# Performance work log

Hardware: AMD Instinct MI355X
Metric: run time of the kernel (lower is better)

Reference implementation:

```python
import jax, jax.numpy as jnp
import numpy as np

B, N_ENC, N_DEC = 32, 512, 512
IN_V, OUT_V = 2000, 2000
H, F, K, P = 256, 256, 5, 4  # P = |G| (indices < P are masked to 0 before embedding)
E_ENC, E_DEC = 128, 128


def setup_inputs() -> dict:
    key = jax.random.key(0)
    ks = jax.random.split(key, 16)
    s = lambda i, shape, scale=0.05: jax.random.normal(ks[i], shape, jnp.float32) * scale
    return dict(
        xs_idx=jax.random.randint(ks[0], (B, N_ENC), 0, IN_V),
        ys_idx=jax.random.randint(ks[1], (B, N_DEC), 0, OUT_V),
        gembed_W=s(2, (IN_V, F)),
        gconv_W=s(3, (K, F, F)),
        gdecode_W=s(4, (F, OUT_V)),
        enc_embed=s(5, (IN_V, E_ENC)),
        dec_embed=s(6, (OUT_V, E_DEC)),
        enc_Wih=s(7, (4 * H, E_ENC)),
        enc_Whh=s(8, (4 * H, H)),
        enc_b=jnp.zeros((4 * H,), jnp.float32),
        dec_Wih=s(9, (4 * H, E_DEC)),
        dec_Whh=s(10, (4 * H, H)),
        dec_b=jnp.zeros((4 * H,), jnp.float32),
        T=jax.random.uniform(ks[11], (H, 2 * H), jnp.float32, -0.5, 0.5),
    )


def _lstm(x, Wih, Whh, b, h0, c0):
    # x: (B, T, D); PyTorch gate order i, f, g, o
    def step(carry, xt):
        h, c = carry
        z = xt @ Wih.T + h @ Whh.T + b
        i, f, g, o = jnp.split(z, 4, axis=-1)
        c = jax.nn.sigmoid(f) * c + jax.nn.sigmoid(i) * jnp.tanh(g)
        h = jax.nn.sigmoid(o) * jnp.tanh(c)
        return (h, c), h
    (hT, cT), hs = jax.lax.scan(step, (h0, c0), jnp.swapaxes(x, 0, 1))
    return jnp.swapaxes(hs, 0, 1), hT, cT


def reference(xs_idx, ys_idx, gembed_W, gconv_W, gdecode_W, enc_embed, dec_embed,
              enc_Wih, enc_Whh, enc_b, dec_Wih, dec_Whh, dec_b, T):
    # --- G-equivariant stack: per-encoder-position distribution over output vocab ---
    e = jnp.tanh(gembed_W[xs_idx])  # (B, Ne, F)
    c = jax.lax.conv_general_dilated(e, gconv_W, (1,), 'SAME',
                                     dimension_numbers=('NWC', 'WIO', 'NWC'))
    probs = jax.nn.softmax(jnp.tanh(c) @ gdecode_W, axis=-1)  # (B, Ne, V)
    # encoder_scores[b, i, j] = probs[b, i, ys[b, j]]
    idx = jnp.broadcast_to(ys_idx[:, None, :], (probs.shape[0], probs.shape[1], ys_idx.shape[1]))
    encoder_scores = jnp.take_along_axis(probs, idx, axis=2)  # (B, Ne, Nd)

    # --- invariant LSTM encoder (indices < |G| masked to 0) ---
    xm = jnp.where(xs_idx < P, 0, xs_idx)
    x_embed = enc_embed[xm]  # (B, Ne, E)
    z = jnp.zeros((x_embed.shape[0], H), jnp.float32)
    henc, hT, cT = _lstm(x_embed, enc_Wih, enc_Whh, enc_b, z, z)
    hback, _, _ = _lstm(jnp.flip(x_embed, axis=1), enc_Wih, enc_Whh, enc_b, z, z)
    hback = jnp.flip(hback, axis=1)

    # --- decoder LSTM, initialized with encoder final state ---
    ym = jnp.where(ys_idx < P, 0, ys_idx)
    y_embed = dec_embed[ym]
    out, _, _ = _lstm(y_embed, dec_Wih, dec_Whh, dec_b, hT, cT)
    h_dec = jnp.concatenate([henc[:, -1:, :], out], axis=1)[:, :-1, :]  # (B, Nd, H)
    h_enc = jnp.concatenate([henc, hback], axis=2)  # (B, Ne, 2H)

    # --- bilinear alignment scores: eij[b, i, j] = h_dec[b, j] . (T @ h_enc[b, i]) ---
    Th = jnp.einsum('he,bie->bih', T, h_enc)           # (B, Ne, H)
    eij = jnp.einsum('bjh,bih->bij', h_dec, Th)        # (B, Ne, Nd)
    align = jax.nn.softmax(eij, axis=1)                # softmax over encoder positions

    p = jnp.sum(jnp.log(jnp.sum(encoder_scores * align, axis=1)), axis=1)  # (B,)
    return -jnp.sum(p)
```

## Files before the change

kernel.cpp:

```cpp
#include <hip/hip_runtime.h>

typedef _Float16 f16;
typedef _Float16 f16x2 __attribute__((ext_vector_type(2)));
typedef _Float16 f16x4 __attribute__((ext_vector_type(4)));
typedef _Float16 f16x8 __attribute__((ext_vector_type(8)));
typedef float    f32x4 __attribute__((ext_vector_type(4)));
typedef int      i32x4 __attribute__((ext_vector_type(4)));
typedef unsigned int u32;
typedef unsigned short u16;

#define DEVI static __device__ __forceinline__

static constexpr int LDT = 40;
static constexpr int LDA = 264;

DEVI float sigf(float x){ return 1.f/(1.f + __expf(-x)); }
DEVI float tanh_c(float x){
  x = fminf(fmaxf(x, -15.f), 15.f);
  float e = __expf(2.f*x);
  return (e - 1.f)/(e + 1.f);
}
DEVI float sig_f(float x){ return __builtin_amdgcn_rcpf(1.f + __expf(-x)); }
DEVI float tanh_f(float x){ return 1.f - 2.f*__builtin_amdgcn_rcpf(1.f + __expf(2.f*x)); }
DEVI float wmax16(float v){
  #pragma unroll
  for (int m=1;m<16;m<<=1) v = fmaxf(v, __shfl_xor(v, m, 64));
  return v;
}
DEVI float wsum16(float v){
  #pragma unroll
  for (int m=1;m<16;m<<=1) v += __shfl_xor(v, m, 64);
  return v;
}
DEVI f16x8 frag_ld(const f16* p){ return *(const f16x8*)p; }
DEVI void stage_tileh(int t256, const f16* src, int ld, f16* dst){
  int row = t256>>2, qq = t256&3;
  *(f16x8*)(dst + row*LDT + qq*8) = *(const f16x8*)(src + (size_t)row*ld + qq*8);
}
#define ZERO4(acc) { f32x4 _z = {0.f,0.f,0.f,0.f}; acc[0]=_z; acc[1]=_z; acc[2]=_z; acc[3]=_z; }

DEVI void gemm64h(int t256, const f16* A, int lda, const f16* Bm, int ldb, int K,
                  f16* lA, f16* lB, f32x4 acc[4]){
  const int lane = t256 & 63, wv = t256 >> 6;
  const int l15 = lane & 15, kq = lane >> 4;
  for (int k0=0; k0<K; k0+=32){
    __syncthreads();
    stage_tileh(t256, A + k0, lda, lA);
    stage_tileh(t256, Bm + k0, ldb, lB);
    __syncthreads();
    f16x8 af = frag_ld(lA + (16*wv + l15)*LDT + kq*8);
    #pragma unroll
    for (int nt=0; nt<4; nt++){
      f16x8 bf = frag_ld(lB + (16*nt + l15)*LDT + kq*8);
      acc[nt] = __builtin_amdgcn_mfma_f32_16x16x32_f16(af, bf, acc[nt], 0,0,0);
    }
  }
}

__global__ void k_cvt(const float* __restrict__ s, f16* __restrict__ d, int n){
  int i = blockIdx.x*256 + threadIdx.x;
  if (i < n) d[i] = (f16)s[i];
}
__global__ void k_gconvT(const float* __restrict__ s, f16* __restrict__ d){
  int id = blockIdx.x;
  int fo = threadIdx.x;
  d[(size_t)fo*1280 + id] = (f16)s[(size_t)id*256 + fo];
}
__global__ void k_gdecT(const float* __restrict__ s, f16* __restrict__ d){
  int v = blockIdx.x, f = threadIdx.x;
  f16 val = (f16)0.f;
  if (v < 2000) val = (f16)s[(size_t)f*2000 + v];
  d[(size_t)v*256 + f] = val;
}
__global__ void k_epad(const int* __restrict__ xs, const float* __restrict__ gemb, f16* __restrict__ epad){
  int id = blockIdx.x;
  int f = threadIdx.x;
  int b = id / 516, p = id % 516;
  float v = 0.f;
  if (p >= 2 && p < 514){ int idx = xs[b*512 + p - 2]; v = tanh_c(gemb[(size_t)idx*256 + f]); }
  epad[(size_t)id*256 + f] = (f16)v;
}
__global__ void k_embx(const int* __restrict__ xs, const int* __restrict__ ys,
                       const float* __restrict__ eemb, const float* __restrict__ demb,
                       f16* __restrict__ xo, f16* __restrict__ yo){
  int id = blockIdx.x; int f = threadIdx.x;
  bool dec = id >= 32*512; int id2 = dec ? id - 32*512 : id;
  int idx = dec ? ys[id2] : xs[id2];
  if (idx < 4) idx = 0;
  const float* src = (dec ? demb : eemb) + (size_t)idx*128;
  (dec ? yo : xo)[(size_t)id2*128 + f] = (f16)src[f];
}

__global__ void k_wmax(const float* __restrict__ Whh, u32* __restrict__ ws){
  int i = (blockIdx.x*256 + threadIdx.x)*4;
  float m = 0.f;
  #pragma unroll
  for (int j=0;j<4;j++) m = fmaxf(m, fabsf(Whh[i+j]));
  #pragma unroll
  for (int d=1; d<64; d<<=1) m = fmaxf(m, __shfl_xor(m, d, 64));
  if ((threadIdx.x & 63) == 0) atomicMax(ws, __float_as_uint(m));
}
__global__ void k_wq8(const float* __restrict__ Whh, const u32* __restrict__ ws,
                      i32x4* __restrict__ Wq){
  const int bid = blockIdx.x;
  const int l = threadIdx.x;
  const int kt = bid & 3, t8 = (bid >> 2) & 7, w = bid >> 5;
  const int r15 = l & 15;
  const int u4 = r15 >> 2, g = r15 & 3;
  const int unit = w*32 + t8*4 + u4;
  const int row = g*256 + unit;
  const int k0  = kt*64 + (l >> 4)*16;
  const float scale = 127.f / __uint_as_float(ws[0]);
  int dw[4];
  #pragma unroll
  for (int d=0; d<4; d++){
    u32 acc = 0;
    #pragma unroll
    for (int j=0; j<4; j++){
      float q = __builtin_rintf(Whh[(size_t)row*256 + k0 + d*4 + j] * scale);
      int qi = (int)fminf(fmaxf(q, -127.f), 127.f);
      acc |= ((u32)qi & 0xffu) << (8*j);
    }
    dw[d] = (int)acc;
  }
  i32x4 v = { dw[0], dw[1], dw[2], dw[3] };
  Wq[(size_t)bid*64 + l] = v;
}

__global__ __launch_bounds__(256,4) void k_conv(const f16* __restrict__ epad, const f16* __restrict__ gcT, f16* __restrict__ tf){
  __shared__ f16 lA[64*LDT], lB[64*LDT];
  const int m0 = blockIdx.x*64, n0 = blockIdx.y*64;
  const int b = m0 >> 9, n = m0 & 511;
  f32x4 acc[4]; ZERO4(acc);
  gemm64h(threadIdx.x, epad + ((size_t)b*516 + n)*256, 256, gcT + (size_t)n0*1280, 1280, 1280, lA, lB, acc);
  const int lane=threadIdx.x&63, wv=threadIdx.x>>6, l15=lane&15, kq=lane>>4;
  #pragma unroll
  for (int nt=0;nt<4;nt++)
    #pragma unroll
    for (int r=0;r<4;r++)
      tf[(size_t)(m0 + 16*wv + 4*kq + r)*256 + n0 + nt*16 + l15] = (f16)tanh_c(acc[nt][r]);
}

DEVI void ku_body(int t256, int m0, int n0, const f16* X, const f16* Wih,
                  const float* bias, f16* U, f16* lA, f16* lB){
  f32x4 acc[4]; ZERO4(acc);
  gemm64h(t256, X + (size_t)m0*128, 128, Wih + (size_t)n0*128, 128, 128, lA, lB, acc);
  const int lane=t256&63, wv=t256>>6, l15=lane&15, kq=lane>>4;
  #pragma unroll
  for (int nt=0;nt<4;nt++){
    int n = n0 + nt*16 + l15;
    float bv = bias[n];
    int cnew = (n & 255)*4 + (n >> 8);
    #pragma unroll
    for (int r=0;r<4;r++)
      U[(size_t)(m0 + 16*wv + 4*kq + r)*1024 + cnew] = (f16)(acc[nt][r] + bv);
  }
}

__global__ __launch_bounds__(256,4) void k_u(const f16* __restrict__ X, const f16* __restrict__ Wih,
                                             const float* __restrict__ bias, f16* __restrict__ U){
  __shared__ f16 lA[64*LDT], lB[64*LDT];
  ku_body(threadIdx.x, blockIdx.x*64, blockIdx.y*64, X, Wih, bias, U, lA, lB);
}

DEVI void th_body(int t256, int m0, int n0, const f16* henh, const f16* Tf, f16* Th,
                  f16* lA, f16* lB){
  f32x4 acc[4]; ZERO4(acc);
  gemm64h(t256, henh + (size_t)m0*512, 512, Tf + (size_t)n0*512, 512, 512, lA, lB, acc);
  const int lane=t256&63, wv=t256>>6, l15=lane&15, kq=lane>>4;
  #pragma unroll
  for (int nt=0;nt<4;nt++)
    #pragma unroll
    for (int r=0;r<4;r++)
      Th[(size_t)(m0 + 16*wv + 4*kq + r)*256 + n0 + nt*16 + l15] = (f16)acc[nt][r];
}

DEVI void pass1_body(int tid, int mt, int ns, const f16* tf, const f16* gdT,
                     float* mxp, float* sep, f16* lA, f16* lB2, float* mxs2, float* ses2){
  const int half = tid >> 8, t256 = tid & 255;
  const int lane = tid & 63, wv = t256 >> 6, l15 = lane & 15, kq = lane >> 4;
  f16* lB = lB2 + half*(64*LDT);
  {
    const f16* A = tf + (size_t)mt*64*256;
    int row = tid >> 3, c8 = tid & 7;
    #pragma unroll
    for (int q=0;q<4;q++)
      *(f16x8*)(lA + row*LDA + c8*32 + q*8) = *(const f16x8*)(A + (size_t)row*256 + c8*32 + q*8);
  }
  if (t256 < 64){ mxs2[half*64 + t256] = -1e30f; ses2[half*64 + t256] = 0.f; }
  __syncthreads();
  for (int nci=0; nci<4; nci++){
    const int nc = half*4 + nci;
    const int nbase = ns*512 + nc*64;
    const f16* Bm = gdT + (size_t)nbase*256;
    f32x4 acc[4]; ZERO4(acc);
    for (int k0=0; k0<256; k0+=32){
      __syncthreads();
      stage_tileh(t256, Bm + k0, 256, lB);
      __syncthreads();
      f16x8 af = frag_ld(lA + (16*wv + l15)*LDA + k0 + kq*8);
      #pragma unroll
      for (int nt=0; nt<4; nt++){
        f16x8 bf = frag_ld(lB + (16*nt + l15)*LDT + kq*8);
        acc[nt] = __builtin_amdgcn_mfma_f32_16x16x32_f16(af, bf, acc[nt], 0,0,0);
      }
    }
    #pragma unroll
    for (int r=0;r<4;r++){
      float av[4]; float cm = -1e30f;
      #pragma unroll
      for (int nt=0;nt<4;nt++){
        int gcol = nbase + nt*16 + l15;
        float a = (gcol < 2000) ? acc[nt][r] : -1e30f;
        av[nt] = a; cm = fmaxf(cm, a);
      }
      cm = wmax16(cm);
      int rr = half*64 + 16*wv + 4*kq + r;
      float old = mxs2[rr];
      float nm = fmaxf(old, cm);
      float ss = 0.f;
      #pragma unroll
      for (int nt=0;nt<4;nt++) ss += __expf(av[nt] - nm);
      ss = wsum16(ss);
      if (l15 == 0){
        ses2[rr] = ses2[rr]*__expf(old - nm) + ss;
        mxs2[rr] = nm;
      }
    }
  }
  __syncthreads();
  if (tid < 64){
    float m0 = mxs2[tid], m1 = mxs2[64+tid];
    float nm = fmaxf(m0, m1);
    float se = ses2[tid]*__expf(m0-nm) + ses2[64+tid]*__expf(m1-nm);
    mxp[(size_t)ns*16384 + mt*64 + tid] = nm;
    sep[(size_t)ns*16384 + mt*64 + tid] = se;
  }
}

__global__ void k_comb1(const float* __restrict__ mxp, const float* __restrict__ sep,
                        float* __restrict__ mx, float* __restrict__ se){
  int m = blockIdx.x*256 + threadIdx.x;
  float best = -1e30f;
  #pragma unroll
  for (int k=0;k<4;k++) best = fmaxf(best, mxp[(size_t)k*16384 + m]);
  float s = 0.f;
  #pragma unroll
  for (int k=0;k<4;k++) s += sep[(size_t)k*16384 + m] * __expf(mxp[(size_t)k*16384 + m] - best);
  mx[m] = best; se[m] = s;
}

DEVI void pass2_body(int t256, int it, int jt, int b, const f16* tf, const f16* gdT,
                     const int* ys, const float* mx, const float* se, f16* scT,
                     f16* lA, f16* lB, int* jv){
  const int lane=t256&63, wv=t256>>6, l15=lane&15, kq=lane>>4;
  if (t256<64) jv[t256] = ys[b*512 + jt*64 + t256];
  const f16* A = tf + ((size_t)b*512 + it*64)*256;
  f32x4 acc[4]; ZERO4(acc);
  for (int k0=0;k0<256;k0+=32){
    __syncthreads();
    stage_tileh(t256, A + k0, 256, lA);
    { int row=t256>>2, qq=t256&3;
      *(f16x8*)(lB + row*LDT + qq*8) = *(const f16x8*)(gdT + (size_t)jv[row]*256 + k0 + qq*8); }
    __syncthreads();
    f16x8 af = frag_ld(lA + (16*wv+l15)*LDT + kq*8);
    #pragma unroll
    for (int nt=0;nt<4;nt++){
      f16x8 bf = frag_ld(lB + (16*nt+l15)*LDT + kq*8);
      acc[nt] = __builtin_amdgcn_mfma_f32_16x16x32_f16(af, bf, acc[nt], 0,0,0);
    }
  }
  float mxv[4], rsev[4];
  #pragma unroll
  for (int r=0;r<4;r++){
    int i_ = it*64 + 16*wv + 4*kq + r;
    mxv[r] = mx[b*512 + i_];
    rsev[r] = 1.f / se[b*512 + i_];
  }
  #pragma unroll
  for (int nt=0;nt<4;nt++){
    int j_ = jt*64 + nt*16 + l15;
    #pragma unroll
    for (int r=0;r<4;r++){
      int i_ = it*64 + 16*wv + 4*kq + r;
      scT[((size_t)b*512 + j_)*512 + i_] = (f16)(__expf(acc[nt][r] - mxv[r]) * rsev[r]);
    }
  }
}

__global__ __launch_bounds__(256,2) void k_final(const f16* __restrict__ hdec, const f16* __restrict__ Th,
                                                 const f16* __restrict__ scT,
                                                 float* __restrict__ pmx, float* __restrict__ pden, float* __restrict__ pnum){
  __shared__ f16 lA[64*LDA];
  __shared__ f16 lB[64*LDT];
  __shared__ float mx_s[64], den_s[64], num_s[64];
  const int is = blockIdx.x, jt = blockIdx.y, b = blockIdx.z;
  const int tid = threadIdx.x, lane=tid&63, wv=tid>>6, l15=lane&15, kq=lane>>4;
  {
    const f16* A = hdec + ((size_t)b*512 + jt*64)*256;
    int row = tid>>2, qq = tid&3;
    #pragma unroll
    for (int c=0;c<8;c++)
      *(f16x8*)(lA + row*LDA + c*32 + qq*8) = *(const f16x8*)(A + (size_t)row*256 + c*32 + qq*8);
  }
  if (tid<64){ mx_s[tid]=-1e30f; den_s[tid]=0.f; num_s[tid]=0.f; }
  __syncthreads();
  for (int ic=0; ic<4; ic++){
    const int i0 = is*256 + ic*64;
    const f16* Bm = Th + ((size_t)b*512 + i0)*256;
    f32x4 acc[4]; ZERO4(acc);
    for (int k0=0;k0<256;k0+=32){
      __syncthreads();
      stage_tileh(tid, Bm + k0, 256, lB);
      __syncthreads();
      f16x8 af = frag_ld(lA + (16*wv+l15)*LDA + k0 + kq*8);
      #pragma unroll
      for (int nt=0;nt<4;nt++){
        f16x8 bf = frag_ld(lB + (16*nt+l15)*LDT + kq*8);
        acc[nt] = __builtin_amdgcn_mfma_f32_16x16x32_f16(af, bf, acc[nt], 0,0,0);
      }
    }
    #pragma unroll
    for (int r=0;r<4;r++){
      int jl = 16*wv + 4*kq + r;
      float av[4]; float cm=-1e30f;
      #pragma unroll
      for (int nt=0;nt<4;nt++){ av[nt]=acc[nt][r]; cm=fmaxf(cm,av[nt]); }
      cm = wmax16(cm);
      float old = mx_s[jl], nm = fmaxf(old, cm);
      float ds=0.f, nsum=0.f;
      const size_t srow = ((size_t)b*512 + jt*64 + jl)*512;
      #pragma unroll
      for (int nt=0;nt<4;nt++){
        float e = __expf(av[nt]-nm);
        float sc = (float)scT[srow + i0 + nt*16 + l15];
        ds += e; nsum += sc*e;
      }
      ds = wsum16(ds); nsum = wsum16(nsum);
      if (l15==0){
        float fac = __expf(old-nm);
        den_s[jl] = den_s[jl]*fac + ds;
        num_s[jl] = num_s[jl]*fac + nsum;
        mx_s[jl] = nm;
      }
    }
  }
  __syncthreads();
  if (tid<64){
    size_t idx = (((size_t)b*512) + jt*64 + tid)*2 + is;
    pmx[idx]=mx_s[tid]; pden[idx]=den_s[tid]; pnum[idx]=num_s[tid];
  }
}

__global__ void k_comb2(const float* __restrict__ pmx, const float* __restrict__ pden,
                        const float* __restrict__ pnum, float* __restrict__ out){
  const int b = blockIdx.x, j = threadIdx.x;
  size_t base = ((size_t)b*512 + j)*2;
  float m0=pmx[base], m1=pmx[base+1];
  float m = fmaxf(m0,m1);
  float e0=__expf(m0-m), e1=__expf(m1-m);
  float den = pden[base]*e0 + pden[base+1]*e1;
  float num = pnum[base]*e0 + pnum[base+1]*e1;
  float lp = __logf(num) - __logf(den);
  __shared__ float red[512];
  red[j] = lp;
  __syncthreads();
  for (int st=256; st>0; st>>=1){ if (j<st) red[j]+=red[j+st]; __syncthreads(); }
  if (j==0) atomicAdd(out, -red[0]);
}

DEVI void lstm_core(char* smem, const f16* U, const i32x4* Wq, const u32* ws,
                    u16* hout, float* hTcT, u16* hdec0, int nsteps, int mode, int bid)
{
  char* h8b = smem;
  const int tid = threadIdx.x;
  const int lane = tid & 63, w = tid >> 6;
  const int l15 = lane & 15, kq = lane >> 4;
  const int s = l15 & 3, p = l15 >> 2;
  const int uA = w*32 + 8*p + kq;
  const int uB = uA + 4;

  int dir = 0, b0;
  if (mode == 0){ dir = bid >> 3; b0 = (bid & 7)*4; }
  else b0 = bid*4;

  const float zscale = __uint_as_float(ws[0]) * (1.f/(127.f*127.f));

  i32x4 aw[32];
  #pragma unroll
  for (int f=0; f<32; f++) aw[f] = Wq[(size_t)(w*32 + f)*64 + lane];

  float cA = 0.f, cB = 0.f;
  if (mode == 0){
    ((u32*)h8b)[tid] = 0u;
  } else {
    const float* hp = hTcT + (size_t)(b0+s)*512;
    float hA = hp[uA], hB = hp[uB];
    cA = hp[256 + uA]; cB = hp[256 + uB];
    h8b[((uA>>4)*4 + s)*16 + (uA&15)] = (char)(int)__builtin_rintf(hA*127.f);
    h8b[((uB>>4)*4 + s)*16 + (uB&15)] = (char)(int)__builtin_rintf(hB*127.f);
  }

  const f16* Urow = U + (size_t)(b0+s)*512*1024;
  f16x4 uvA, uvB;
  {
    int tp0 = dir ? (nsteps-1) : 0;
    uvA = *(const f16x4*)(Urow + (size_t)tp0*1024 + uA*4);
    uvB = *(const f16x4*)(Urow + (size_t)tp0*1024 + uB*4);
  }
  __syncthreads();

  int cur = 0;
  #pragma unroll 1
  for (int t=0; t<nsteps; ++t){
    const int tpos = dir ? (nsteps-1-t) : t;
    int tn = dir ? (nsteps-2-t >= 0 ? nsteps-2-t : 0) : (t+1 < nsteps ? t+1 : nsteps-1);
    f16x4 puA = *(const f16x4*)(Urow + (size_t)tn*1024 + uA*4);
    f16x4 puB = *(const f16x4*)(Urow + (size_t)tn*1024 + uB*4);

    const char* hc = h8b + cur*1024;
    i32x4 bf[4];
    #pragma unroll
    for (int kt=0; kt<4; kt++)
      bf[kt] = *(const i32x4*)(hc + ((kt*4 + kq)*4 + s)*16);

    i32x4 acc[8];
    #pragma unroll
    for (int t8=0; t8<8; t8++){
      i32x4 d = {0,0,0,0};
      #pragma unroll
      for (int kt=0; kt<4; kt++)
        d = __builtin_amdgcn_mfma_i32_16x16x64_i8(aw[t8*4+kt], bf[kt], d, 0,0,0);
      acc[t8] = d;
    }

    i32x4 vA, vB;
    #pragma unroll
    for (int e=0; e<4; e++){
      int x0 = (p&1) ? acc[2][e] : acc[0][e];
      int x1 = (p&1) ? acc[6][e] : acc[4][e];
      vA[e] = (p&2) ? x1 : x0;
      int y0 = (p&1) ? acc[3][e] : acc[1][e];
      int y1 = (p&1) ? acc[7][e] : acc[5][e];
      vB[e] = (p&2) ? y1 : y0;
    }

    float hA_, hB_;
    {
      float z0 = fmaf((float)vA[0], zscale, (float)uvA[0]);
      float z1 = fmaf((float)vA[1], zscale, (float)uvA[1]);
      float z2 = fmaf((float)vA[2], zscale, (float)uvA[2]);
      float z3 = fmaf((float)vA[3], zscale, (float)uvA[3]);
      cA = sig_f(z1)*cA + sig_f(z0)*tanh_f(z2);
      hA_ = sig_f(z3)*tanh_f(cA);
    }
    {
      float z0 = fmaf((float)vB[0], zscale, (float)uvB[0]);
      float z1 = fmaf((float)vB[1], zscale, (float)uvB[1]);
      float z2 = fmaf((float)vB[2], zscale, (float)uvB[2]);
      float z3 = fmaf((float)vB[3], zscale, (float)uvB[3]);
      cB = sig_f(z1)*cB + sig_f(z0)*tanh_f(z2);
      hB_ = sig_f(z3)*tanh_f(cB);
    }

    const int nxt = cur ^ 1;
    char* hn = h8b + nxt*1024;
    hn[((uA>>4)*4 + s)*16 + (uA&15)] = (char)(int)__builtin_rintf(hA_*127.f);
    hn[((uB>>4)*4 + s)*16 + (uB&15)] = (char)(int)__builtin_rintf(hB_*127.f);

    f16 fA = (f16)hA_, fB = (f16)hB_;
    if (mode == 0){
      u16* hr = hout + ((size_t)(b0+s)*512 + tpos)*512 + dir*256;
      hr[uA] = __builtin_bit_cast(u16, fA);
      hr[uB] = __builtin_bit_cast(u16, fB);
      if (!dir && t == nsteps-1){
        hdec0[(size_t)(b0+s)*512*256 + uA] = __builtin_bit_cast(u16, fA);
        hdec0[(size_t)(b0+s)*512*256 + uB] = __builtin_bit_cast(u16, fB);
        float* hp = hTcT + (size_t)(b0+s)*512;
        hp[uA] = hA_; hp[uB] = hB_;
        hp[256+uA] = cA; hp[256+uB] = cB;
      }
    } else {
      u16* hr = hout + ((size_t)(b0+s)*512 + (t+1))*256;
      hr[uA] = __builtin_bit_cast(u16, fA);
      hr[uB] = __builtin_bit_cast(u16, fB);
    }

    asm volatile("s_waitcnt lgkmcnt(0)" ::: "memory");
    __builtin_amdgcn_s_barrier();
    asm volatile("" ::: "memory");
    __builtin_amdgcn_sched_barrier(0);

    cur = nxt;
    uvA = puA; uvB = puB;
  }
}

__global__ __launch_bounds__(512,2) void k_mega_enc(
    const f16* __restrict__ Uenc, const i32x4* __restrict__ Wqe, const u32* __restrict__ wse,
    u16* __restrict__ henh, float* __restrict__ hTcT, u16* __restrict__ hdec0,
    const f16* __restrict__ tf, const f16* __restrict__ gdT,
    float* __restrict__ mxp, float* __restrict__ sep,
    const f16* __restrict__ yemb, const f16* __restrict__ Wihd,
    const float* __restrict__ db, f16* __restrict__ Udec)
{
  __shared__ __align__(16) char smem[45056];
  const int bid = blockIdx.x;
  const int tid = threadIdx.x;
  if (bid < 16){
    lstm_core(smem, Uenc, Wqe, wse, henh, hTcT, hdec0, 512, 0, bid);
  } else if (bid < 1040){
    int vb = bid - 16;
    int mt = vb >> 2;
    int ns = vb & 3;
    pass1_body(tid, mt, ns, tf, gdT, mxp, sep,
               (f16*)smem, (f16*)(smem + 33792), (float*)(smem + 44032), (float*)(smem + 44544));
  } else {
    int vb = bid - 1040;
    int half = tid >> 8, t256 = tid & 255;
    int vbm = vb >> 4, ny = vb & 15;
    int m0 = (vbm*2 + half)*64;
    int n0 = ny*64;
    char* base = smem + half*10240;
    ku_body(t256, m0, n0, yemb, Wihd, db, Udec, (f16*)base, (f16*)(base + 5120));
  }
}

__global__ __launch_bounds__(512,2) void k_mega_dec(
    const f16* __restrict__ Udec, const i32x4* __restrict__ Wqd, const u32* __restrict__ wsd,
    u16* __restrict__ hdec, float* __restrict__ hTcT,
    const f16* __restrict__ tf, const f16* __restrict__ gdT, const int* __restrict__ ys,
    const float* __restrict__ mx, const float* __restrict__ se, f16* __restrict__ scT,
    const f16* __restrict__ henh, const f16* __restrict__ Tf, f16* __restrict__ Th)
{
  __shared__ __align__(16) char smem[24576];
  const int bid = blockIdx.x;
  const int tid = threadIdx.x;
  if (bid < 8){
    lstm_core(smem, Udec, Wqd, wsd, hdec, hTcT, hdec, 511, 1, bid);
  } else if (bid < 1032){
    int vb = bid - 8;
    int half = tid >> 8, t256 = tid & 255;
    int b = vb >> 5, rem = vb & 31;
    int jt = rem >> 2, it = (rem & 3)*2 + half;
    char* base = smem + half*10496;
    pass2_body(t256, it, jt, b, tf, gdT, ys, mx, se, scT,
               (f16*)base, (f16*)(base + 5120), (int*)(base + 10240));
  } else {
    int vb = bid - 1032;
    int half = tid >> 8, t256 = tid & 255;
    int m0 = ((vb >> 2)*2 + half)*64;
    int n0 = (vb & 3)*64;
    char* base = smem + half*10240;
    th_body(t256, m0, n0, henh, Tf, Th, (f16*)base, (f16*)(base + 5120));
  }
}

extern "C" void kernel_launch(void* const* d_in, const int* in_sizes, int n_in,
                              void* d_out, int out_size, void* d_ws, size_t ws_size,
                              hipStream_t stream)
{
  (void)in_sizes; (void)n_in; (void)out_size;
  const int*   xs    = (const int*)d_in[0];
  const int*   ys    = (const int*)d_in[1];
  const float* gemb  = (const float*)d_in[2];
  const float* gconv = (const float*)d_in[3];
  const float* gdec  = (const float*)d_in[4];
  const float* eemb  = (const float*)d_in[5];
  const float* demb  = (const float*)d_in[6];
  const float* eWih  = (const float*)d_in[7];
  const float* eWhh  = (const float*)d_in[8];
  const float* eb    = (const float*)d_in[9];
  const float* dWih  = (const float*)d_in[10];
  const float* dWhh  = (const float*)d_in[11];
  const float* db    = (const float*)d_in[12];
  const float* Tm    = (const float*)d_in[13];

  char* wsb = (char*)d_ws;
  size_t off = 0;
  auto take = [&](size_t bytes)->char*{ char* p = wsb + off; off += (bytes + 255) & ~(size_t)255; return p; };
  f16* epad  = (f16*)take((size_t)32*516*256*2);
  f16* tf    = (f16*)take((size_t)32*512*256*2);
  f16* xemb  = (f16*)take((size_t)32*512*128*2);
  f16* yemb  = (f16*)take((size_t)32*512*128*2);
  f16* Uenc  = (f16*)take((size_t)32*512*1024*2);
  f16* Udec  = (f16*)take((size_t)32*512*1024*2);
  f16* henh  = (f16*)take((size_t)32*512*512*2);
  f16* hdec  = (f16*)take((size_t)32*512*256*2);
  f16* Th    = (f16*)take((size_t)32*512*256*2);
  f16* scT   = (f16*)take((size_t)32*512*512*2);
  float* mx  = (float*)take((size_t)16384*4);
  float* se  = (float*)take((size_t)16384*4);
  float* mxp = (float*)take((size_t)4*16384*4);
  float* sep = (float*)take((size_t)4*16384*4);
  float* pmx = (float*)take((size_t)32*512*2*4);
  float* pden= (float*)take((size_t)32*512*2*4);
  float* pnum= (float*)take((size_t)32*512*2*4);
  float* hTcT= (float*)take((size_t)32*512*4);
  f16* Wihe  = (f16*)take((size_t)1024*128*2);
  f16* Wihd  = (f16*)take((size_t)1024*128*2);
  f16* Tf    = (f16*)take((size_t)256*512*2);
  f16* gcT   = (f16*)take((size_t)256*1280*2);
  f16* gdT   = (f16*)take((size_t)2048*256*2);
  i32x4* Wq8e = (i32x4*)take((size_t)256*64*16);
  i32x4* Wq8d = (i32x4*)take((size_t)256*64*16);
  u32* wsc   = (u32*)take(8);
  if (off > ws_size) return;

  hipMemsetAsync(d_out, 0, sizeof(float), stream);
  hipMemsetAsync(wsc, 0, 8, stream);

  k_cvt<<<dim3(512),  256, 0, stream>>>(eWih, Wihe, 1024*128);
  k_cvt<<<dim3(512),  256, 0, stream>>>(dWih, Wihd, 1024*128);
  k_cvt<<<dim3(512),  256, 0, stream>>>(Tm,   Tf,   256*512);
  k_gconvT<<<dim3(1280), 256, 0, stream>>>(gconv, gcT);
  k_gdecT <<<dim3(2048), 256, 0, stream>>>(gdec, gdT);
  k_wmax<<<dim3(256), 256, 0, stream>>>(eWhh, wsc + 0);
  k_wmax<<<dim3(256), 256, 0, stream>>>(dWhh, wsc + 1);
  k_wq8<<<dim3(256), 64, 0, stream>>>(eWhh, wsc + 0, Wq8e);
  k_wq8<<<dim3(256), 64, 0, stream>>>(dWhh, wsc + 1, Wq8d);
  k_epad<<<dim3(32*516), 256, 0, stream>>>(xs, gemb, epad);
  k_embx<<<dim3(2*32*512), 128, 0, stream>>>(xs, ys, eemb, demb, xemb, yemb);

  k_conv<<<dim3(256,4), 256, 0, stream>>>(epad, gcT, tf);
  k_u<<<dim3(256,16), 256, 0, stream>>>(xemb, Wihe, eb, Uenc);

  k_mega_enc<<<dim3(3088), 512, 0, stream>>>(Uenc, Wq8e, wsc + 0, (u16*)henh, hTcT, (u16*)hdec,
                                             tf, gdT, mxp, sep, yemb, Wihd, db, Udec);
  k_comb1<<<dim3(64), 256, 0, stream>>>(mxp, sep, mx, se);

  k_mega_dec<<<dim3(1544), 512, 0, stream>>>(Udec, Wq8d, wsc + 1, (u16*)hdec, hTcT,
                                             tf, gdT, ys, mx, se, scT, henh, Tf, Th);

  k_final<<<dim3(2,8,32), 256, 0, stream>>>(hdec, Th, scT, pmx, pden, pnum);
  k_comb2<<<dim3(32), 512, 0, stream>>>(pmx, pden, pnum, (float*)d_out);
}
```

Baseline: 1.136 ms.

## Convert mega kernels' side work to persistent grid-stride workers

Both fused kernels now launch 512 blocks instead of thousands, and non-LSTM blocks loop over the pass1/ku and pass2/th work items with a grid stride. Blocks 256..271 (enc) and 256..263 (dec) exit early, apparently so the side workers avoid sharing CUs with the latency-critical LSTM blocks. The aim is to cut block dispatch overhead and interference with the serial LSTM recurrence. The cost is less parallel slack and possible tail imbalance among the fixed set of workers.

Result: no change. 1.134 ms (-0.2%).

```diff
diff --git a/kernel.cpp b/kernel.cpp
--- a/kernel.cpp
+++ b/kernel.cpp
@@ -509,20 +509,26 @@
   const int tid = threadIdx.x;
   if (bid < 16){
     lstm_core(smem, Uenc, Wqe, wse, henh, hTcT, hdec0, 512, 0, bid);
-  } else if (bid < 1040){
-    int vb = bid - 16;
-    int mt = vb >> 2;
-    int ns = vb & 3;
-    pass1_body(tid, mt, ns, tf, gdT, mxp, sep,
-               (f16*)smem, (f16*)(smem + 33792), (float*)(smem + 44032), (float*)(smem + 44544));
-  } else {
-    int vb = bid - 1040;
-    int half = tid >> 8, t256 = tid & 255;
-    int vbm = vb >> 4, ny = vb & 15;
-    int m0 = (vbm*2 + half)*64;
-    int n0 = ny*64;
-    char* base = smem + half*10240;
-    ku_body(t256, m0, n0, yemb, Wihd, db, Udec, (f16*)base, (f16*)(base + 5120));
+    return;
+  }
+  if (bid >= 256 && bid < 272) return;
+  const int w = (bid < 256) ? (bid - 16) : (bid - 32);
+  for (int v = w; v < 3072; v += 480){
+    __syncthreads();
+    if (v < 1024){
+      int mt = v >> 2;
+      int ns = v & 3;
+      pass1_body(tid, mt, ns, tf, gdT, mxp, sep,
+                 (f16*)smem, (f16*)(smem + 33792), (float*)(smem + 44032), (float*)(smem + 44544));
+    } else {
+      int vb = v - 1024;
+      int half = tid >> 8, t256 = tid & 255;
+      int vbm = vb >> 4, ny = vb & 15;
+      int m0 = (vbm*2 + half)*64;
+      int n0 = ny*64;
+      char* base = smem + half*10240;
+      ku_body(t256, m0, n0, yemb, Wihd, db, Udec, (f16*)base, (f16*)(base + 5120));
+    }
   }
 }
 
@@ -538,21 +544,27 @@
   const int tid = threadIdx.x;
   if (bid < 8){
     lstm_core(smem, Udec, Wqd, wsd, hdec, hTcT, hdec, 511, 1, bid);
-  } else if (bid < 1032){
-    int vb = bid - 8;
-    int half = tid >> 8, t256 = tid & 255;
-    int b = vb >> 5, rem = vb & 31;
-    int jt = rem >> 2, it = (rem & 3)*2 + half;
-    char* base = smem + half*10496;
-    pass2_body(t256, it, jt, b, tf, gdT, ys, mx, se, scT,
-               (f16*)base, (f16*)(base + 5120), (int*)(base + 10240));
-  } else {
-    int vb = bid - 1032;
-    int half = tid >> 8, t256 = tid & 255;
-    int m0 = ((vb >> 2)*2 + half)*64;
-    int n0 = (vb & 3)*64;
-    char* base = smem + half*10240;
-    th_body(t256, m0, n0, henh, Tf, Th, (f16*)base, (f16*)(base + 5120));
+    return;
+  }
+  if (bid >= 256 && bid < 264) return;
+  const int w = (bid < 256) ? (bid - 8) : (bid - 16);
+  for (int v = w; v < 1536; v += 496){
+    __syncthreads();
+    if (v < 1024){
+      int half = tid >> 8, t256 = tid & 255;
+      int b = v >> 5, rem = v & 31;
+      int jt = rem >> 2, it = (rem & 3)*2 + half;
+      char* base = smem + half*10496;
+      pass2_body(t256, it, jt, b, tf, gdT, ys, mx, se, scT,
+                 (f16*)base, (f16*)(base + 5120), (int*)(base + 10240));
+    } else {
+      int vb = v - 1024;
+      int half = tid >> 8, t256 = tid & 255;
+      int m0 = ((vb >> 2)*2 + half)*64;
+      int n0 = (vb & 3)*64;
+      char* base = smem + half*10240;
+      th_body(t256, m0, n0, henh, Tf, Th, (f16*)base, (f16*)(base + 5120));
+    }
   }
 }
 
@@ -625,12 +637,12 @@
   k_conv<<<dim3(256,4), 256, 0, stream>>>(epad, gcT, tf);
   k_u<<<dim3(256,16), 256, 0, stream>>>(xemb, Wihe, eb, Uenc);
 
-  k_mega_enc<<<dim3(3088), 512, 0, stream>>>(Uenc, Wq8e, wsc + 0, (u16*)henh, hTcT, (u16*)hdec,
-                                             tf, gdT, mxp, sep, yemb, Wihd, db, Udec);
+  k_mega_enc<<<dim3(512), 512, 0, stream>>>(Uenc, Wq8e, wsc + 0, (u16*)henh, hTcT, (u16*)hdec,
+                                            tf, gdT, mxp, sep, yemb, Wihd, db, Udec);
   k_comb1<<<dim3(64), 256, 0, stream>>>(mxp, sep, mx, se);
 
-  k_mega_dec<<<dim3(1544), 512, 0, stream>>>(Udec, Wq8d, wsc + 1, (u16*)hdec, hTcT,
-                                             tf, gdT, ys, mx, se, scT, henh, Tf, Th);
+  k_mega_dec<<<dim3(512), 512, 0, stream>>>(Udec, Wq8d, wsc + 1, (u16*)hdec, hTcT,
+                                            tf, gdT, ys, mx, se, scT, henh, Tf, Th);
 
   k_final<<<dim3(2,8,32), 256, 0, stream>>>(hdec, Th, scT, pmx, pden, pnum);
   k_comb2<<<dim3(32), 512, 0, stream>>>(pmx, pden, pnum, (float*)d_out);
```
